# Kernel optimization log

Hardware: AMD Instinct MI355X
Metric: run time of the kernel (lower is better)

## Reference

```python
import jax, jax.numpy as jnp
import numpy as np

IN_FEATURES = 512
OUT_FEATURES = 128
KERNEL_DIM = 32
BATCH = 128


def setup_inputs() -> dict:
    key = jax.random.key(0)
    kx, kT = jax.random.split(key)
    x = jax.random.normal(kx, (BATCH, IN_FEATURES), dtype=jnp.float32)
    # nn.Parameter initialized with normal(0, 1)
    T = jax.random.normal(kT, (IN_FEATURES, OUT_FEATURES, KERNEL_DIM), dtype=jnp.float32)
    return {"x": x, "T": T}


def reference(x, T):
    B = x.shape[0]
    in_f, out_f, k_dim = T.shape
    # projection: [B, in] @ [in, out*k] -> [B, out, k]
    m = (x @ T.reshape(in_f, out_f * k_dim)).reshape(B, out_f, k_dim)
    # pairwise L1 distance over kernel dim: [B, B, out]
    # original: M = m[None], M_T = m[:, None]; norm = |M - M_T|.sum(3); o_b = exp(-norm).sum(0) - 1
    norm = jnp.abs(m[None, :, :, :] - m[:, None, :, :]).sum(axis=-1)  # [i=B, j=B, out]
    o_b = jnp.exp(-norm).sum(axis=0) - 1.0  # [B, out] (subtract self-distance term exp(0)=1)
    return jnp.concatenate([x, o_b], axis=1)  # [B, in + out]
```

## Files before the change

### kernel.cpp

```cpp
#include <hip/hip_runtime.h>

#define B_SZ    128
#define IN_F    512
#define OUT_F   128
#define NC      4096
#define KD      32
#define OUT_COLS 640
#define MO_PITCH 36

typedef __attribute__((ext_vector_type(8))) short  bf16x8;
typedef __attribute__((ext_vector_type(4))) float  f32x4;

union FragAB { unsigned int u[4]; bf16x8 s; };

static __device__ __forceinline__ unsigned int pack2(float lo, float hi) {
    return (__float_as_uint(lo) >> 16) | (__float_as_uint(hi) & 0xFFFF0000u);
}

__global__ __launch_bounds__(256, 2) void gemm_kernel(
    const float* __restrict__ x,
    const float* __restrict__ T,
    float* __restrict__ m)
{
    const int tid  = threadIdx.x;
    const int lane = tid & 63;
    const int w    = tid >> 6;
    const int n0   = (blockIdx.x * 4 + w) * 16;
    const int m0   = blockIdx.y * 16;
    const int col  = lane & 15;
    const int q    = lane >> 4;

    const float* xrow = x + (m0 + col) * IN_F;
    f32x4 acc = {0.f, 0.f, 0.f, 0.f};

    #pragma unroll 4
    for (int kt = 0; kt < 16; ++kt) {
        const int k0 = kt * 32 + q * 8;
        const float4 a0 = *(const float4*)(xrow + k0);
        const float4 a1 = *(const float4*)(xrow + k0 + 4);
        FragAB af;
        af.u[0] = pack2(a0.x, a0.y); af.u[1] = pack2(a0.z, a0.w);
        af.u[2] = pack2(a1.x, a1.y); af.u[3] = pack2(a1.z, a1.w);
        const float* tb = T + (size_t)k0 * NC + n0 + col;
        const float b0 = tb[0*NC], b1 = tb[1*NC], b2 = tb[2*NC], b3 = tb[3*NC];
        const float b4 = tb[4*NC], b5 = tb[5*NC], b6 = tb[6*NC], b7 = tb[7*NC];
        FragAB bf;
        bf.u[0] = pack2(b0, b1); bf.u[1] = pack2(b2, b3);
        bf.u[2] = pack2(b4, b5); bf.u[3] = pack2(b6, b7);
        acc = __builtin_amdgcn_mfma_f32_16x16x32_bf16(af.s, bf.s, acc, 0, 0, 0);
    }
    float* dst = m + (size_t)(m0 + q * 4) * NC + n0 + col;
    dst[0*NC] = acc[0]; dst[1*NC] = acc[1]; dst[2*NC] = acc[2]; dst[3*NC] = acc[3];
}

__global__ __launch_bounds__(1024, 4) void pairwise_kernel(
    const float* __restrict__ x,
    const float* __restrict__ m,
    float* __restrict__ out)
{
    __shared__ float mo[B_SZ * MO_PITCH];
    __shared__ float psum[64 * 16];

    const int tid   = threadIdx.x;
    const int o     = blockIdx.x >> 1;
    const int jhalf = blockIdx.x & 1;

    if (tid < 64) {
        int idx = blockIdx.x * 64 + tid;
        int b = idx >> 7, c4 = idx & 127;
        float4 v = ((const float4*)x)[idx];
        *(float4*)(out + b * OUT_COLS + c4 * 4) = v;
    }

    {
        const int b = tid >> 3, k4 = tid & 7;
        float4 v = *(const float4*)(m + (size_t)b * NC + o * KD + k4 * 4);
        *(float4*)&mo[b * MO_PITCH + k4 * 4] = v;
    }
    __syncthreads();

    const int jj  = tid & 63;
    const int isl = tid >> 6;
    const int j   = jhalf * 64 + jj;

    float mj[KD];
    #pragma unroll
    for (int k4 = 0; k4 < 8; ++k4) {
        float4 v = *(const float4*)&mo[j * MO_PITCH + k4 * 4];
        mj[k4*4+0] = v.x; mj[k4*4+1] = v.y; mj[k4*4+2] = v.z; mj[k4*4+3] = v.w;
    }

    float s = 0.f;
    const int i0 = isl * 8;
    for (int i = i0; i < i0 + 8; ++i) {
        float norm = 0.f;
        #pragma unroll
        for (int k4 = 0; k4 < 8; ++k4) {
            float4 v = *(const float4*)&mo[i * MO_PITCH + k4 * 4];
            norm += fabsf(mj[k4*4+0] - v.x) + fabsf(mj[k4*4+1] - v.y)
                  + fabsf(mj[k4*4+2] - v.z) + fabsf(mj[k4*4+3] - v.w);
        }
        s += __expf(-norm);
    }
    psum[jj * 16 + isl] = s;
    __syncthreads();
    if (tid < 64) {
        float tot = 0.f;
        #pragma unroll
        for (int u = 0; u < 16; ++u) tot += psum[tid * 16 + u];
        out[(jhalf * 64 + tid) * OUT_COLS + IN_F + o] = tot - 1.0f;
    }
}

extern "C" void kernel_launch(void* const* d_in, const int* in_sizes, int n_in,
                              void* d_out, int out_size, void* d_ws, size_t ws_size,
                              hipStream_t stream) {
    const float* x = (const float*)d_in[0];
    const float* T = (const float*)d_in[1];
    float* out = (float*)d_out;
    float* m = (float*)d_ws;

    gemm_kernel<<<dim3(64, 8), 256, 0, stream>>>(x, T, m);
    pairwise_kernel<<<256, 1024, 0, stream>>>(x, m, out);
}
```

Before: 76.88 us.

## Tile GEMM through LDS with bf16 pre-converted x and separate prep kernel

Adds a prep kernel that copies x into the output and converts x to bf16 in workspace. The GEMM now stages 64x128 tiles of x and 128x32 tiles of T through shared memory, transposing and converting T to bf16 on the way in, so global loads are coalesced and reused across waves. The goal is to replace the old strided scalar T loads, which were issued per lane. In exchange it adds a third kernel launch, uses fewer and larger blocks (256 blocks of 512 threads), and the bf16 shared-memory stores of T may bank-conflict.

```diff
diff --git a/kernel.cpp b/kernel.cpp
--- a/kernel.cpp
+++ b/kernel.cpp
@@ -7,54 +7,83 @@
 #define KD      32
 #define OUT_COLS 640
 #define MO_PITCH 36
+#define AS_PITCH 136
+#define BK      128
 
 typedef __attribute__((ext_vector_type(8))) short  bf16x8;
 typedef __attribute__((ext_vector_type(4))) float  f32x4;
 
-union FragAB { unsigned int u[4]; bf16x8 s; };
-
-static __device__ __forceinline__ unsigned int pack2(float lo, float hi) {
-    return (__float_as_uint(lo) >> 16) | (__float_as_uint(hi) & 0xFFFF0000u);
+static __device__ __forceinline__ unsigned short f2bfu(float f) {
+    return (unsigned short)(__float_as_uint(f) >> 16);
 }
 
-__global__ __launch_bounds__(256, 2) void gemm_kernel(
-    const float* __restrict__ x,
+__global__ __launch_bounds__(256) void prep_kernel(
+    const float* __restrict__ x, float* __restrict__ out,
+    unsigned short* __restrict__ xb)
+{
+    int idx = blockIdx.x * 256 + threadIdx.x;
+    int b = idx >> 7, c4 = idx & 127;
+    float4 v = ((const float4*)x)[idx];
+    *(float4*)(out + b * OUT_COLS + c4 * 4) = v;
+    ushort4 w;
+    w.x = f2bfu(v.x); w.y = f2bfu(v.y); w.z = f2bfu(v.z); w.w = f2bfu(v.w);
+    *(ushort4*)(xb + idx * 4) = w;
+}
+
+__global__ __launch_bounds__(512, 2) void gemm_kernel(
+    const unsigned short* __restrict__ xb,
     const float* __restrict__ T,
     float* __restrict__ m)
 {
+    __shared__ unsigned short as[64 * AS_PITCH];
+    __shared__ unsigned short bs[32 * AS_PITCH];
+
     const int tid  = threadIdx.x;
     const int lane = tid & 63;
     const int w    = tid >> 6;
-    const int n0   = (blockIdx.x * 4 + w) * 16;
-    const int m0   = blockIdx.y * 16;
     const int col  = lane & 15;
     const int q    = lane >> 4;
+    const int n0   = blockIdx.x * 32;
+    const int m0   = blockIdx.y * 64;
+    const int mt   = w >> 1, nt = w & 1;
 
-    const float* xrow = x + (m0 + col) * IN_F;
     f32x4 acc = {0.f, 0.f, 0.f, 0.f};
 
-    #pragma unroll 4
-    for (int kt = 0; kt < 16; ++kt) {
-        const int k0 = kt * 32 + q * 8;
-        const float4 a0 = *(const float4*)(xrow + k0);
-        const float4 a1 = *(const float4*)(xrow + k0 + 4);
-        FragAB af;
-        af.u[0] = pack2(a0.x, a0.y); af.u[1] = pack2(a0.z, a0.w);
-        af.u[2] = pack2(a1.x, a1.y); af.u[3] = pack2(a1.z, a1.w);
-        const float* tb = T + (size_t)k0 * NC + n0 + col;
-        const float b0 = tb[0*NC], b1 = tb[1*NC], b2 = tb[2*NC], b3 = tb[3*NC];
-        const float b4 = tb[4*NC], b5 = tb[5*NC], b6 = tb[6*NC], b7 = tb[7*NC];
-        FragAB bf;
-        bf.u[0] = pack2(b0, b1); bf.u[1] = pack2(b2, b3);
-        bf.u[2] = pack2(b4, b5); bf.u[3] = pack2(b6, b7);
-        acc = __builtin_amdgcn_mfma_f32_16x16x32_bf16(af.s, bf.s, acc, 0, 0, 0);
+    for (int k0 = 0; k0 < IN_F; k0 += BK) {
+        __syncthreads();
+        #pragma unroll
+        for (int p = 0; p < 2; ++p) {
+            int u = tid + p * 512;
+            int row = u >> 4, o8 = u & 15;
+            uint4 v = *(const uint4*)(xb + (m0 + row) * IN_F + k0 + o8 * 8);
+            *(uint4*)&as[row * AS_PITCH + o8 * 8] = v;
+        }
+        #pragma unroll
+        for (int p = 0; p < 2; ++p) {
+            int u = tid + p * 512;
+            int kk = u >> 3, nq = u & 7;
+            float4 v = *(const float4*)(T + (size_t)(k0 + kk) * NC + n0 + nq * 4);
+            int nb = nq * 4;
+            bs[(nb + 0) * AS_PITCH + kk] = f2bfu(v.x);
+            bs[(nb + 1) * AS_PITCH + kk] = f2bfu(v.y);
+            bs[(nb + 2) * AS_PITCH + kk] = f2bfu(v.z);
+            bs[(nb + 3) * AS_PITCH + kk] = f2bfu(v.w);
+        }
+        __syncthreads();
+        #pragma unroll
+        for (int kt = 0; kt < 4; ++kt) {
+            const int krel = kt * 32 + q * 8;
+            bf16x8 af = *(const bf16x8*)&as[(mt * 16 + col) * AS_PITCH + krel];
+            bf16x8 bf = *(const bf16x8*)&bs[(nt * 16 + col) * AS_PITCH + krel];
+            acc = __builtin_amdgcn_mfma_f32_16x16x32_bf16(af, bf, acc, 0, 0, 0);
+        }
     }
-    float* dst = m + (size_t)(m0 + q * 4) * NC + n0 + col;
-    dst[0*NC] = acc[0]; dst[1*NC] = acc[1]; dst[2*NC] = acc[2]; dst[3*NC] = acc[3];
+    float* dst = m + (size_t)(m0 + mt * 16 + q * 4) * NC + n0 + nt * 16 + col;
+    dst[0 * NC] = acc[0]; dst[1 * NC] = acc[1];
+    dst[2 * NC] = acc[2]; dst[3 * NC] = acc[3];
 }
 
 __global__ __launch_bounds__(1024, 4) void pairwise_kernel(
-    const float* __restrict__ x,
     const float* __restrict__ m,
     float* __restrict__ out)
 {
@@ -64,13 +93,6 @@
     const int tid   = threadIdx.x;
     const int o     = blockIdx.x >> 1;
     const int jhalf = blockIdx.x & 1;
-
-    if (tid < 64) {
-        int idx = blockIdx.x * 64 + tid;
-        int b = idx >> 7, c4 = idx & 127;
-        float4 v = ((const float4*)x)[idx];
-        *(float4*)(out + b * OUT_COLS + c4 * 4) = v;
-    }
 
     {
         const int b = tid >> 3, k4 = tid & 7;
@@ -119,7 +141,9 @@
     const float* T = (const float*)d_in[1];
     float* out = (float*)d_out;
     float* m = (float*)d_ws;
+    unsigned short* xb = (unsigned short*)((char*)d_ws + (2u << 20));
 
-    gemm_kernel<<<dim3(64, 8), 256, 0, stream>>>(x, T, m);
-    pairwise_kernel<<<256, 1024, 0, stream>>>(x, m, out);
+    prep_kernel<<<64, 256, 0, stream>>>(x, out, xb);
+    gemm_kernel<<<dim3(128, 2), 512, 0, stream>>>(xb, T, m);
+    pairwise_kernel<<<256, 1024, 0, stream>>>(m, out);
 }
```

Result: faster. 72.87 us (-5.2%).
